# Kernel tuning notes

Hardware: AMD Instinct MI355X
Metric: run time of the kernel (lower is better)

## Reference

```python
import jax, jax.numpy as jnp
import numpy as np

N_NODES = 50000
N_GRAPHS = 64
NEG_SLOPE = 0.2


def gat_conv(x, src, dst, W, a_src, a_dst, b, n_nodes, concat):
    """PyG-style GATConv (eval mode, self-loops already in src/dst).
    x: [N, Fin], W: [Fin, H*C], a_src/a_dst: [H, C], b: [H*C] or [C].
    """
    H, C = a_src.shape
    h = (x @ W).reshape(n_nodes, H, C)                      # [N,H,C]
    al_src = jnp.einsum('nhc,hc->nh', h, a_src)             # [N,H]
    al_dst = jnp.einsum('nhc,hc->nh', h, a_dst)             # [N,H]
    e = jax.nn.leaky_relu(al_src[src] + al_dst[dst], NEG_SLOPE)  # [E,H]
    # softmax over incoming edges per destination node
    m = jax.ops.segment_max(e, dst, num_segments=n_nodes)   # [N,H]
    ex = jnp.exp(e - m[dst])
    s = jax.ops.segment_sum(ex, dst, num_segments=n_nodes)  # [N,H]
    alpha = ex / (s[dst] + 1e-16)                           # [E,H]
    # attention-weighted aggregation of source features
    out = jax.ops.segment_sum(h[src] * alpha[..., None], dst, num_segments=n_nodes)  # [N,H,C]
    out = out.reshape(n_nodes, H * C) if concat else out.mean(axis=1)
    return out + b


def setup_inputs() -> dict:
    key = jax.random.key(0)
    ks = jax.random.split(key, 12)
    n, e = N_NODES, 800000
    x = jax.random.normal(ks[0], (n, 500), dtype=jnp.float32)
    edge_index = jax.random.randint(ks[1], (2, e), 0, n, dtype=jnp.int64)
    batch = jnp.sort(jax.random.randint(ks[2], (n,), 0, N_GRAPHS, dtype=jnp.int64))
    hid, heads = 64, 4
    sc = 0.1
    W1 = jax.random.normal(ks[3], (500, heads * hid), dtype=jnp.float32) * sc
    a_src1 = jax.random.normal(ks[4], (heads, hid), dtype=jnp.float32) * sc
    a_dst1 = jax.random.normal(ks[5], (heads, hid), dtype=jnp.float32) * sc
    b1 = jnp.zeros((heads * hid,), dtype=jnp.float32)
    W2 = jax.random.normal(ks[6], (heads * hid, hid), dtype=jnp.float32) * sc
    a_src2 = jax.random.normal(ks[7], (1, hid), dtype=jnp.float32) * sc
    a_dst2 = jax.random.normal(ks[8], (1, hid), dtype=jnp.float32) * sc
    b2 = jnp.zeros((hid,), dtype=jnp.float32)
    Wl = jax.random.normal(ks[9], (hid, 2), dtype=jnp.float32) * sc
    bl = jnp.zeros((2,), dtype=jnp.float32)
    return dict(x=x, edge_index=edge_index, batch=batch,
                W1=W1, a_src1=a_src1, a_dst1=a_dst1, b1=b1,
                W2=W2, a_src2=a_src2, a_dst2=a_dst2, b2=b2,
                Wl=Wl, bl=bl)


def reference(x, edge_index, batch, W1, a_src1, a_dst1, b1,
              W2, a_src2, a_dst2, b2, Wl, bl):
    n = x.shape[0]
    # PyG GATConv adds self-loops by default
    loops = jnp.arange(n, dtype=edge_index.dtype)
    src = jnp.concatenate([edge_index[0], loops])
    dst = jnp.concatenate([edge_index[1], loops])
    h = jax.nn.relu(gat_conv(x, src, dst, W1, a_src1, a_dst1, b1, n, concat=True))
    h = jax.nn.relu(gat_conv(h, src, dst, W2, a_src2, a_dst2, b2, n, concat=False))
    # global mean pool over graphs
    sums = jax.ops.segment_sum(h, batch, num_segments=N_GRAPHS)      # [G, hid]
    cnt = jax.ops.segment_sum(jnp.ones((n,), h.dtype), batch, num_segments=N_GRAPHS)
    pooled = sums / jnp.maximum(cnt, 1.0)[:, None]
    return pooled @ Wl + bl                                          # [G, 2]
```

## Files before the change

### kernel.cpp

```cpp
#include <hip/hip_runtime.h>
#include <math.h>

#define NN   50000
#define NE   800000
#define NET  850000
#define NG   64
#define KIN  500
#define NEG  0.2f

typedef unsigned short ushort_t;
typedef __attribute__((ext_vector_type(8))) short bf8_t;
typedef __attribute__((ext_vector_type(8))) unsigned short us8_t;
typedef __attribute__((ext_vector_type(4))) float f4_t;

__device__ __forceinline__ float bf2f(ushort_t u) {
    unsigned v = ((unsigned)u) << 16;
    return __builtin_bit_cast(float, v);
}
__device__ __forceinline__ ushort_t f2bf(float f) {
    unsigned b = __builtin_bit_cast(unsigned, f);
    unsigned r = (b + 0x7FFFu + ((b >> 16) & 1u)) >> 16;
    return (ushort_t)r;
}

#define GLOAD_LDS(g, l)                                                        \
    __builtin_amdgcn_global_load_lds(                                          \
        (const __attribute__((address_space(1))) unsigned int*)(g),            \
        (__attribute__((address_space(3))) unsigned int*)(l), 16, 0, 0)

__global__ void k_deg(const int* __restrict__ ei, int* __restrict__ deg) {
    int e = blockIdx.x * 256 + threadIdx.x;
    if (e >= NET) return;
    int dst = (e < NE) ? ei[NE + e] : (e - NE);
    atomicAdd(&deg[dst], 1);
}

__global__ void k_scan_part(const int* __restrict__ deg, int* __restrict__ part) {
    __shared__ int s[256];
    int t = threadIdx.x;
    int i = blockIdx.x * 256 + t;
    s[t] = (i < NN) ? deg[i] : 0;
    __syncthreads();
    for (int off = 128; off > 0; off >>= 1) {
        if (t < off) s[t] += s[t + off];
        __syncthreads();
    }
    if (t == 0) part[blockIdx.x] = s[0];
}

__global__ void k_scan_top(int* __restrict__ part, int nb) {
    __shared__ int s[256];
    int t = threadIdx.x;
    int v = (t < nb) ? part[t] : 0;
    s[t] = v;
    __syncthreads();
    for (int off = 1; off < 256; off <<= 1) {
        int a = (t >= off) ? s[t - off] : 0;
        __syncthreads();
        s[t] += a;
        __syncthreads();
    }
    if (t < nb) part[t] = s[t] - v;
}

__global__ void k_scan_apply(const int* __restrict__ deg, const int* __restrict__ part,
                             int* __restrict__ rowptr) {
    __shared__ int s[256];
    int t = threadIdx.x;
    int i = blockIdx.x * 256 + t;
    int v = (i < NN) ? deg[i] : 0;
    s[t] = v;
    __syncthreads();
    for (int off = 1; off < 256; off <<= 1) {
        int a = (t >= off) ? s[t - off] : 0;
        __syncthreads();
        s[t] += a;
        __syncthreads();
    }
    if (i < NN) rowptr[i] = part[blockIdx.x] + s[t] - v;
    if (i == 0) rowptr[NN] = NET;
}

__global__ void k_fill(const int* __restrict__ ei, const int* __restrict__ rowptr,
                       int* __restrict__ cursor, int* __restrict__ csr) {
    int e = blockIdx.x * 256 + threadIdx.x;
    if (e >= NET) return;
    int src, dst;
    if (e < NE) { src = ei[e]; dst = ei[NE + e]; }
    else        { src = dst = e - NE; }
    int pos = atomicAdd(&cursor[dst], 1);
    csr[rowptr[dst] + pos] = src;
}

__global__ void k_cast_x(const float* __restrict__ x, ushort_t* __restrict__ xb) {
    int idx = blockIdx.x * 256 + threadIdx.x;
    if (idx >= 50048 * 128) return;
    int row = idx >> 7, k4 = (idx & 127) * 4;
    ushort4 o = make_ushort4(0, 0, 0, 0);
    if (row < NN && k4 < KIN) {
        float4 v = *(const float4*)&x[(size_t)row * KIN + k4];
        o.x = f2bf(v.x); o.y = f2bf(v.y); o.z = f2bf(v.z); o.w = f2bf(v.w);
    }
    *(ushort4*)&xb[(size_t)idx * 4] = o;
}

template <int KSRC, int KPAD, int NOUT>
__global__ void k_cast_wt(const float* __restrict__ W, ushort_t* __restrict__ Wt) {
    int idx = blockIdx.x * 256 + threadIdx.x;
    if (idx >= NOUT * KPAD) return;
    int n = idx / KPAD, k = idx - n * KPAD;
    float v = (k < KSRC) ? W[(size_t)k * NOUT + n] : 0.f;
    Wt[idx] = f2bf(v);
}

template <int K, int LDA, int BM, int BN, int WM, int FOUT, int HEADS>
__global__ __launch_bounds__(256) void k_mfma(
    const ushort_t* __restrict__ A, const ushort_t* __restrict__ Wt,
    const float* __restrict__ a_s, const float* __restrict__ a_d,
    ushort_t* __restrict__ Hb, float* __restrict__ als, float* __restrict__ ald)
{
    __shared__ __align__(16) ushort_t lA[BM * 32];
    __shared__ __align__(16) ushort_t lB[BN * 32];
    const int t    = threadIdx.x;
    const int row0 = blockIdx.y * BM;
    const int n0   = blockIdx.x * BN;
    const int ww   = t >> 6, lane = t & 63;
    const int wm   = ww % WM, wn = ww / WM;
    const int lrow = lane & 15, lq = lane >> 4;

    f4_t acc[4][4] = {};

    for (int k0 = 0; k0 < K; k0 += 32) {
#pragma unroll
        for (int i = 0; i < BM / 64; i++) {
            int c = i * 256 + t;
            int row = c >> 2, kq = c & 3;
            const ushort_t* gp = A + (size_t)(row0 + row) * LDA + k0 + kq * 8;
            GLOAD_LDS(gp, &lA[c * 8]);
        }
#pragma unroll
        for (int i = 0; i < BN / 64; i++) {
            int c = i * 256 + t;
            int row = c >> 2, kq = c & 3;
            const ushort_t* gp = Wt + (size_t)(n0 + row) * K + k0 + kq * 8;
            GLOAD_LDS(gp, &lB[c * 8]);
        }
        __syncthreads();
        bf8_t af[4], bfr[4];
#pragma unroll
        for (int i = 0; i < 4; i++)
            af[i] = *(const bf8_t*)&lA[(wm * 64 + i * 16 + lrow) * 32 + lq * 8];
#pragma unroll
        for (int j = 0; j < 4; j++)
            bfr[j] = *(const bf8_t*)&lB[(wn * 64 + j * 16 + lrow) * 32 + lq * 8];
#pragma unroll
        for (int i = 0; i < 4; i++)
#pragma unroll
            for (int j = 0; j < 4; j++)
                acc[i][j] = __builtin_amdgcn_mfma_f32_16x16x32_bf16(af[i], bfr[j], acc[i][j], 0, 0, 0);
        __syncthreads();
    }

    const int head = (n0 + wn * 64) >> 6;
    float as4[4], ad4[4];
#pragma unroll
    for (int j = 0; j < 4; j++) {
        as4[j] = a_s[head * 64 + j * 16 + lrow];
        ad4[j] = a_d[head * 64 + j * 16 + lrow];
    }
#pragma unroll
    for (int i = 0; i < 4; i++) {
#pragma unroll
        for (int r = 0; r < 4; r++) {
            int row = row0 + wm * 64 + i * 16 + lq * 4 + r;
            float v0 = acc[i][0][r], v1 = acc[i][1][r], v2 = acc[i][2][r], v3 = acc[i][3][r];
            if (row < NN) {
                size_t base = (size_t)row * FOUT + n0 + wn * 64 + lrow;
                Hb[base +  0] = f2bf(v0);
                Hb[base + 16] = f2bf(v1);
                Hb[base + 32] = f2bf(v2);
                Hb[base + 48] = f2bf(v3);
            }
            float ps = v0 * as4[0] + v1 * as4[1] + v2 * as4[2] + v3 * as4[3];
            float pd = v0 * ad4[0] + v1 * ad4[1] + v2 * ad4[2] + v3 * ad4[3];
#pragma unroll
            for (int off = 1; off < 16; off <<= 1) {
                ps += __shfl_xor(ps, off);
                pd += __shfl_xor(pd, off);
            }
            if (lrow == 0 && row < NN) {
                als[(size_t)row * HEADS + head] = ps;
                ald[(size_t)row * HEADS + head] = pd;
            }
        }
    }
}

__global__ __launch_bounds__(256) void k_agg1(
    const int* __restrict__ rowptr, const int* __restrict__ csr,
    const ushort_t* __restrict__ Hb, const float* __restrict__ als,
    const float* __restrict__ ald, const float* __restrict__ bias,
    ushort_t* __restrict__ OutB)
{
    int w = threadIdx.x >> 6, lane = threadIdx.x & 63;
    int dst = blockIdx.x * 4 + w;
    if (dst >= NN) return;
    const int slot = lane >> 5;
    const int head = (lane >> 3) & 3;
    const int f0   = (lane & 7) * 8;
    const int beg = rowptr[dst], end = rowptr[dst + 1];
    const float adst = ald[dst * 4 + head];

    int  i      = beg;
    int  e_idx  = i + slot;
    bool valid  = e_idx < end;
    int  src    = csr[valid ? e_idx : (end - 1)];
    float as_v  = als[src * 4 + head];
    us8_t xv    = *(const us8_t*)&Hb[(size_t)src * 256 + head * 64 + f0];

    float m = -1e30f, s = 0.f;
    float acc[8] = {};
    while (true) {
        int inext = i + 2;
        bool more = inext < end;
        int src2 = 0; float as2 = 0.f; us8_t xv2 = {};
        bool valid2 = false;
        if (more) {
            int e2 = inext + slot;
            valid2 = e2 < end;
            src2 = csr[valid2 ? e2 : (end - 1)];
            as2  = als[src2 * 4 + head];
            xv2  = *(const us8_t*)&Hb[(size_t)src2 * 256 + head * 64 + f0];
        }
        float e = as_v + adst;
        e = (e > 0.f) ? e : NEG * e;
        if (!valid) e = -1e30f;
        float eo = __shfl_xor(e, 32);
        float mn = fmaxf(m, fmaxf(e, eo));
        float sc = __expf(m - mn);
        float pr = __expf(e - mn);
        s = s * sc + pr;
#pragma unroll
        for (int j = 0; j < 8; j++)
            acc[j] = acc[j] * sc + pr * bf2f((ushort_t)xv[j]);
        m = mn;
        if (!more) break;
        i = inext; src = src2; as_v = as2; xv = xv2; valid = valid2;
    }
    s += __shfl_xor(s, 32);
#pragma unroll
    for (int j = 0; j < 8; j++) acc[j] += __shfl_xor(acc[j], 32);
    if (lane < 32) {
        us8_t o8;
#pragma unroll
        for (int j = 0; j < 8; j++) {
            float o = acc[j] / (s + 1e-16f) + bias[head * 64 + f0 + j];
            o = (o > 0.f) ? o : 0.f;
            o8[j] = f2bf(o);
        }
        *(us8_t*)&OutB[(size_t)dst * 256 + head * 64 + f0] = o8;
    }
}

__global__ __launch_bounds__(256) void k_agg2(
    const int* __restrict__ rowptr, const int* __restrict__ csr,
    const ushort_t* __restrict__ Hb, const float* __restrict__ als,
    const float* __restrict__ ald, const float* __restrict__ bias,
    float* __restrict__ OutF)
{
    int w = threadIdx.x >> 6, lane = threadIdx.x & 63;
    int dst = blockIdx.x * 4 + w;
    if (dst >= NN) return;
    const int slot = lane >> 4;
    const int f0   = (lane & 15) * 4;
    const int beg = rowptr[dst], end = rowptr[dst + 1];
    const float adst = ald[dst];

    int  i     = beg;
    int  e_idx = i + slot;
    bool valid = e_idx < end;
    int  src   = csr[valid ? e_idx : (end - 1)];
    float as_v = als[src];
    ushort4 xv = *(const ushort4*)&Hb[(size_t)src * 64 + f0];

    float m = -1e30f, s = 0.f;
    float acc[4] = {};
    while (true) {
        int inext = i + 4;
        bool more = inext < end;
        int src2 = 0; float as2 = 0.f; ushort4 xv2 = make_ushort4(0, 0, 0, 0);
        bool valid2 = false;
        if (more) {
            int e2 = inext + slot;
            valid2 = e2 < end;
            src2 = csr[valid2 ? e2 : (end - 1)];
            as2  = als[src2];
            xv2  = *(const ushort4*)&Hb[(size_t)src2 * 64 + f0];
        }
        float e = as_v + adst;
        e = (e > 0.f) ? e : NEG * e;
        if (!valid) e = -1e30f;
        float e1 = fmaxf(e, __shfl_xor(e, 16));
        float e2m = fmaxf(e1, __shfl_xor(e1, 32));
        float mn = fmaxf(m, e2m);
        float sc = __expf(m - mn);
        float pr = __expf(e - mn);
        s = s * sc + pr;
        acc[0] = acc[0] * sc + pr * bf2f(xv.x);
        acc[1] = acc[1] * sc + pr * bf2f(xv.y);
        acc[2] = acc[2] * sc + pr * bf2f(xv.z);
        acc[3] = acc[3] * sc + pr * bf2f(xv.w);
        m = mn;
        if (!more) break;
        i = inext; src = src2; as_v = as2; xv = xv2; valid = valid2;
    }
    s += __shfl_xor(s, 16); s += __shfl_xor(s, 32);
#pragma unroll
    for (int j = 0; j < 4; j++) {
        acc[j] += __shfl_xor(acc[j], 16);
        acc[j] += __shfl_xor(acc[j], 32);
    }
    if (lane < 16) {
        float4 o;
        float* op = &o.x;
#pragma unroll
        for (int j = 0; j < 4; j++) {
            float v = acc[j] / (s + 1e-16f) + bias[f0 + j];
            op[j] = (v > 0.f) ? v : 0.f;
        }
        *(float4*)&OutF[(size_t)dst * 64 + f0] = o;
    }
}

__global__ void k_pool_final(const float* __restrict__ out2, const int* __restrict__ batch,
                             const float* __restrict__ Wl, const float* __restrict__ bl,
                             float* __restrict__ out)
{
    int g = blockIdx.x;
    int lo, hi;
    { int a = 0, b = NN; while (a < b) { int mm = (a + b) >> 1; if (batch[mm] < g) a = mm + 1; else b = mm; } lo = a; }
    { int a = lo, b = NN; while (a < b) { int mm = (a + b) >> 1; if (batch[mm] < g + 1) a = mm + 1; else b = mm; } hi = a; }
    int t = threadIdx.x, c = t & 63, r = t >> 6;
    float s = 0.f;
    for (int n = lo + r; n < hi; n += 4) s += out2[(size_t)n * 64 + c];
    __shared__ float red[256];
    red[t] = s;
    __syncthreads();
    if (t < 64) {
        float p = red[t] + red[t + 64] + red[t + 128] + red[t + 192];
        int cntv = hi - lo;
        p /= (float)(cntv > 0 ? cntv : 1);
        float r0 = p * Wl[t * 2 + 0];
        float r1 = p * Wl[t * 2 + 1];
#pragma unroll
        for (int off = 32; off > 0; off >>= 1) {
            r0 += __shfl_xor(r0, off);
            r1 += __shfl_xor(r1, off);
        }
        if (t == 0) {
            out[g * 2 + 0] = r0 + bl[0];
            out[g * 2 + 1] = r1 + bl[1];
        }
    }
}

extern "C" void kernel_launch(void* const* d_in, const int* in_sizes, int n_in,
                              void* d_out, int out_size, void* d_ws, size_t ws_size,
                              hipStream_t stream)
{
    const float* x    = (const float*)d_in[0];
    const int*   ei   = (const int*)  d_in[1];
    const int*   batch= (const int*)  d_in[2];
    const float* W1   = (const float*)d_in[3];
    const float* as1  = (const float*)d_in[4];
    const float* ad1  = (const float*)d_in[5];
    const float* b1   = (const float*)d_in[6];
    const float* W2   = (const float*)d_in[7];
    const float* as2  = (const float*)d_in[8];
    const float* ad2  = (const float*)d_in[9];
    const float* b2   = (const float*)d_in[10];
    const float* Wl   = (const float*)d_in[11];
    const float* bl   = (const float*)d_in[12];
    float* out = (float*)d_out;

    int*   deg    = (int*)d_ws;
    int*   cursor = deg + 50048;
    int*   part   = cursor + 50048;
    int*   rowptr = part + 256;
    int*   csr    = rowptr + 50064;
    ushort_t* xb  = (ushort_t*)(csr + 850048);
    ushort_t* Wt1 = xb + (size_t)50048 * 512;
    ushort_t* Wt2 = Wt1 + 131072;
    ushort_t* h1b = Wt2 + 16384;
    float* al1s   = (float*)(h1b + (size_t)50000 * 256);
    float* al1d   = al1s + 200000;
    float* al2s   = al1d + 200000;
    float* al2d   = al2s + 50000;
    ushort_t* out1b = xb;
    ushort_t* h2b   = xb + 13000000;
    float*    out2  = (float*)(xb + 16400000);

    hipMemsetAsync(deg, 0, 2 * 50048 * sizeof(int), stream);

    k_deg       <<<(NET + 255) / 256, 256, 0, stream>>>(ei, deg);
    k_scan_part <<<196, 256, 0, stream>>>(deg, part);
    k_scan_top  <<<1,   256, 0, stream>>>(part, 196);
    k_scan_apply<<<196, 256, 0, stream>>>(deg, part, rowptr);
    k_fill      <<<(NET + 255) / 256, 256, 0, stream>>>(ei, rowptr, cursor, csr);

    k_cast_x<<<(50048 * 128 + 255) / 256, 256, 0, stream>>>(x, xb);
    k_cast_wt<500, 512, 256><<<(256 * 512 + 255) / 256, 256, 0, stream>>>(W1, Wt1);
    k_cast_wt<256, 256, 64> <<<(64 * 256 + 255) / 256, 256, 0, stream>>>(W2, Wt2);

    k_mfma<512, 512, 128, 128, 2, 256, 4><<<dim3(2, 391), 256, 0, stream>>>(
        xb, Wt1, as1, ad1, h1b, al1s, al1d);
    k_agg1<<<(NN + 3) / 4, 256, 0, stream>>>(rowptr, csr, h1b, al1s, al1d, b1, out1b);
    hipMemsetAsync(out1b + (size_t)50000 * 256, 0, (size_t)176 * 256 * sizeof(ushort_t), stream);

    k_mfma<256, 256, 256, 64, 4, 64, 1><<<dim3(1, 196), 256, 0, stream>>>(
        out1b, Wt2, as2, ad2, h2b, al2s, al2d);
    k_agg2<<<(NN + 3) / 4, 256, 0, stream>>>(rowptr, csr, h2b, al2s, al2d, b2, out2);

    k_pool_final<<<NG, 256, 0, stream>>>(out2, batch, Wl, bl, out);
}
```

Before: 497.0 us.

## Split GAT aggregation into softmax pass then plain weighted-sum pass

Both aggregation kernels now compute the per-destination softmax max and sum in a first edge-parallel pass, staging normalized attention weights in shared memory (up to 128 edges). The second pass then does a plain weighted accumulation with no running rescale, removing per-edge exp calls and the serial online-softmax dependency from the feature loop. The cost is an extra pass over csr and als plus shared-memory use, with a recompute fallback for high-degree nodes.

```diff
diff --git a/kernel.cpp b/kernel.cpp
--- a/kernel.cpp
+++ b/kernel.cpp
@@ -196,136 +196,182 @@
     }
 }
 
+#define CAP1 128
 __global__ __launch_bounds__(256) void k_agg1(
     const int* __restrict__ rowptr, const int* __restrict__ csr,
     const ushort_t* __restrict__ Hb, const float* __restrict__ als,
     const float* __restrict__ ald, const float* __restrict__ bias,
     ushort_t* __restrict__ OutB)
 {
+    __shared__ float salpha[4][CAP1 * 4];
     int w = threadIdx.x >> 6, lane = threadIdx.x & 63;
     int dst = blockIdx.x * 4 + w;
     if (dst >= NN) return;
-    const int slot = lane >> 5;
-    const int head = (lane >> 3) & 3;
-    const int f0   = (lane & 7) * 8;
+    float* Aw = salpha[w];
     const int beg = rowptr[dst], end = rowptr[dst + 1];
-    const float adst = ald[dst * 4 + head];
-
-    int  i      = beg;
-    int  e_idx  = i + slot;
-    bool valid  = e_idx < end;
-    int  src    = csr[valid ? e_idx : (end - 1)];
-    float as_v  = als[src * 4 + head];
-    us8_t xv    = *(const us8_t*)&Hb[(size_t)src * 256 + head * 64 + f0];
-
+    const int deg = end - beg;
+
+    const int hd   = lane & 3;
+    const int slot = lane >> 2;
+    const float adst = ald[dst * 4 + hd];
     float m = -1e30f, s = 0.f;
-    float acc[8] = {};
+    for (int k = slot; k < deg; k += 16) {
+        int src = csr[beg + k];
+        float e = als[src * 4 + hd] + adst;
+        e = (e > 0.f) ? e : NEG * e;
+        if (k < CAP1) Aw[k * 4 + hd] = e;
+        float mn = fmaxf(m, e);
+        s = s * __expf(m - mn) + __expf(e - mn);
+        m = mn;
+    }
+#pragma unroll
+    for (int off = 4; off < 64; off <<= 1) {
+        float mo = __shfl_xor(m, off);
+        float so = __shfl_xor(s, off);
+        float mn = fmaxf(m, mo);
+        s = s * __expf(m - mn) + so * __expf(mo - mn);
+        m = mn;
+    }
+    float inv = 1.f / (s + 1e-16f);
+    int cap4 = (deg < CAP1 ? deg : CAP1) * 4;
+    for (int j = lane; j < cap4; j += 64)
+        Aw[j] = __expf(Aw[j] - m) * inv;
+
+    const int slot2 = lane >> 5;
+    const int head2 = (lane >> 3) & 3;
+    const int f0    = (lane & 7) * 8;
+    const float m2  = __shfl(m, head2);
+    const float i2  = __shfl(inv, head2);
+    const float ad2 = __shfl(adst, head2);
+
+    float facc[8] = {};
+    int  k0    = 0;
+    int  ke    = slot2;
+    bool valid = ke < deg;
+    int  src   = csr[beg + (valid ? ke : 0)];
+    us8_t xv   = *(const us8_t*)&Hb[(size_t)src * 256 + head2 * 64 + f0];
     while (true) {
-        int inext = i + 2;
-        bool more = inext < end;
-        int src2 = 0; float as2 = 0.f; us8_t xv2 = {};
-        bool valid2 = false;
+        int k0n = k0 + 2;
+        bool more = k0n < deg;
+        int src2 = 0; us8_t xv2 = {}; bool valid2 = false;
         if (more) {
-            int e2 = inext + slot;
-            valid2 = e2 < end;
-            src2 = csr[valid2 ? e2 : (end - 1)];
-            as2  = als[src2 * 4 + head];
-            xv2  = *(const us8_t*)&Hb[(size_t)src2 * 256 + head * 64 + f0];
-        }
-        float e = as_v + adst;
-        e = (e > 0.f) ? e : NEG * e;
-        if (!valid) e = -1e30f;
-        float eo = __shfl_xor(e, 32);
-        float mn = fmaxf(m, fmaxf(e, eo));
-        float sc = __expf(m - mn);
-        float pr = __expf(e - mn);
-        s = s * sc + pr;
+            int ke2 = k0n + slot2;
+            valid2 = ke2 < deg;
+            src2 = csr[beg + (valid2 ? ke2 : 0)];
+            xv2  = *(const us8_t*)&Hb[(size_t)src2 * 256 + head2 * 64 + f0];
+        }
+        float al;
+        if (ke < CAP1) {
+            al = Aw[ke * 4 + head2];
+        } else {
+            float e = als[src * 4 + head2] + ad2;
+            e = (e > 0.f) ? e : NEG * e;
+            al = __expf(e - m2) * i2;
+        }
+        if (!valid) al = 0.f;
 #pragma unroll
         for (int j = 0; j < 8; j++)
-            acc[j] = acc[j] * sc + pr * bf2f((ushort_t)xv[j]);
-        m = mn;
+            facc[j] += al * bf2f((ushort_t)xv[j]);
         if (!more) break;
-        i = inext; src = src2; as_v = as2; xv = xv2; valid = valid2;
-    }
-    s += __shfl_xor(s, 32);
-#pragma unroll
-    for (int j = 0; j < 8; j++) acc[j] += __shfl_xor(acc[j], 32);
+        k0 = k0n; ke = k0 + slot2; valid = valid2; src = src2; xv = xv2;
+    }
+#pragma unroll
+    for (int j = 0; j < 8; j++) facc[j] += __shfl_xor(facc[j], 32);
     if (lane < 32) {
         us8_t o8;
 #pragma unroll
         for (int j = 0; j < 8; j++) {
-            float o = acc[j] / (s + 1e-16f) + bias[head * 64 + f0 + j];
+            float o = facc[j] + bias[head2 * 64 + f0 + j];
             o = (o > 0.f) ? o : 0.f;
             o8[j] = f2bf(o);
         }
-        *(us8_t*)&OutB[(size_t)dst * 256 + head * 64 + f0] = o8;
-    }
-}
-
+        *(us8_t*)&OutB[(size_t)dst * 256 + head2 * 64 + f0] = o8;
+    }
+}
+
+#define CAP2 128
 __global__ __launch_bounds__(256) void k_agg2(
     const int* __restrict__ rowptr, const int* __restrict__ csr,
     const ushort_t* __restrict__ Hb, const float* __restrict__ als,
     const float* __restrict__ ald, const float* __restrict__ bias,
     float* __restrict__ OutF)
 {
+    __shared__ float salpha2[4][CAP2];
     int w = threadIdx.x >> 6, lane = threadIdx.x & 63;
     int dst = blockIdx.x * 4 + w;
     if (dst >= NN) return;
-    const int slot = lane >> 4;
-    const int f0   = (lane & 15) * 4;
+    float* Aw = salpha2[w];
     const int beg = rowptr[dst], end = rowptr[dst + 1];
+    const int deg = end - beg;
     const float adst = ald[dst];
 
-    int  i     = beg;
-    int  e_idx = i + slot;
-    bool valid = e_idx < end;
-    int  src   = csr[valid ? e_idx : (end - 1)];
-    float as_v = als[src];
+    float m = -1e30f, s = 0.f;
+    for (int k = lane; k < deg; k += 64) {
+        int src = csr[beg + k];
+        float e = als[src] + adst;
+        e = (e > 0.f) ? e : NEG * e;
+        if (k < CAP2) Aw[k] = e;
+        float mn = fmaxf(m, e);
+        s = s * __expf(m - mn) + __expf(e - mn);
+        m = mn;
+    }
+#pragma unroll
+    for (int off = 1; off < 64; off <<= 1) {
+        float mo = __shfl_xor(m, off);
+        float so = __shfl_xor(s, off);
+        float mn = fmaxf(m, mo);
+        s = s * __expf(m - mn) + so * __expf(mo - mn);
+        m = mn;
+    }
+    float inv = 1.f / (s + 1e-16f);
+    int cap = deg < CAP2 ? deg : CAP2;
+    for (int j = lane; j < cap; j += 64)
+        Aw[j] = __expf(Aw[j] - m) * inv;
+
+    const int slot2 = lane >> 4;
+    const int f0    = (lane & 15) * 4;
+    float facc[4] = {};
+    int  k0    = 0;
+    int  ke    = slot2;
+    bool valid = ke < deg;
+    int  src   = csr[beg + (valid ? ke : 0)];
     ushort4 xv = *(const ushort4*)&Hb[(size_t)src * 64 + f0];
-
-    float m = -1e30f, s = 0.f;
-    float acc[4] = {};
     while (true) {
-        int inext = i + 4;
-        bool more = inext < end;
-        int src2 = 0; float as2 = 0.f; ushort4 xv2 = make_ushort4(0, 0, 0, 0);
-        bool valid2 = false;
+        int k0n = k0 + 4;
+        bool more = k0n < deg;
+        int src2 = 0; ushort4 xv2 = make_ushort4(0, 0, 0, 0); bool valid2 = false;
         if (more) {
-            int e2 = inext + slot;
-            valid2 = e2 < end;
-            src2 = csr[valid2 ? e2 : (end - 1)];
-            as2  = als[src2];
+            int ke2 = k0n + slot2;
+            valid2 = ke2 < deg;
+            src2 = csr[beg + (valid2 ? ke2 : 0)];
             xv2  = *(const ushort4*)&Hb[(size_t)src2 * 64 + f0];
         }
-        float e = as_v + adst;
-        e = (e > 0.f) ? e : NEG * e;
-        if (!valid) e = -1e30f;
-        float e1 = fmaxf(e, __shfl_xor(e, 16));
-        float e2m = fmaxf(e1, __shfl_xor(e1, 32));
-        float mn = fmaxf(m, e2m);
-        float sc = __expf(m - mn);
-        float pr = __expf(e - mn);
-        s = s * sc + pr;
-        acc[0] = acc[0] * sc + pr * bf2f(xv.x);
-        acc[1] = acc[1] * sc + pr * bf2f(xv.y);
-        acc[2] = acc[2] * sc + pr * bf2f(xv.z);
-        acc[3] = acc[3] * sc + pr * bf2f(xv.w);
-        m = mn;
+        float al;
+        if (ke < CAP2) al = Aw[ke];
+        else {
+            float e = als[src] + adst;
+            e = (e > 0.f) ? e : NEG * e;
+            al = __expf(e - m) * inv;
+        }
+        if (!valid) al = 0.f;
+        facc[0] += al * bf2f(xv.x);
+        facc[1] += al * bf2f(xv.y);
+        facc[2] += al * bf2f(xv.z);
+        facc[3] += al * bf2f(xv.w);
         if (!more) break;
-        i = inext; src = src2; as_v = as2; xv = xv2; valid = valid2;
-    }
-    s += __shfl_xor(s, 16); s += __shfl_xor(s, 32);
+        k0 = k0n; ke = k0 + slot2; valid = valid2; src = src2; xv = xv2;
+    }
 #pragma unroll
     for (int j = 0; j < 4; j++) {
-        acc[j] += __shfl_xor(acc[j], 16);
-        acc[j] += __shfl_xor(acc[j], 32);
+        facc[j] += __shfl_xor(facc[j], 16);
+        facc[j] += __shfl_xor(facc[j], 32);
     }
     if (lane < 16) {
         float4 o;
         float* op = &o.x;
 #pragma unroll
         for (int j = 0; j < 4; j++) {
-            float v = acc[j] / (s + 1e-16f) + bias[f0 + j];
+            float v = facc[j] + bias[f0 + j];
             op[j] = (v > 0.f) ? v : 0.f;
         }
         *(float4*)&OutF[(size_t)dst * 64 + f0] = o;
```

Measured after the change: 500.2 us. No clear change (+0.7%).
